# Performance work log

Measured on AMD Instinct MI355X. Metric: run time of the kernel, lower is better.

Reference implementation:

```python
import jax, jax.numpy as jnp
import numpy as np
import math

NUM_HEADS = 8


def setup_inputs() -> dict:
    key = jax.random.key(0)
    ks = jax.random.split(key, 6)
    b, s, e = 4, 2048, 512
    x = jax.random.normal(ks[0], (b, s, e), dtype=jnp.float32)
    # 0/1 adjacency matrix as float (it multiplies the scores in the module)
    adj = jax.random.randint(ks[1], (b, s, s), 0, 2).astype(jnp.float32)
    scale = 0.02
    Wqkv_w = jax.random.normal(ks[2], (3 * e, e), dtype=jnp.float32) * scale
    Wqkv_b = jax.random.normal(ks[3], (3 * e,), dtype=jnp.float32) * scale
    out_w = jax.random.normal(ks[4], (e, e), dtype=jnp.float32) * scale
    out_b = jax.random.normal(ks[5], (e,), dtype=jnp.float32) * scale
    return {"x": x, "adj": adj, "Wqkv_w": Wqkv_w, "Wqkv_b": Wqkv_b,
            "out_w": out_w, "out_b": out_b}


def reference(x, adj, Wqkv_w, Wqkv_b, out_w, out_b):
    b, s, e = x.shape
    h = NUM_HEADS
    d = e // h
    # fused qkv projection: (b, s, 3*e) -> (b, s, 3, h, d)
    qkv = (x @ Wqkv_w.T + Wqkv_b).reshape(b, s, 3, h, d)
    qkv = jnp.transpose(qkv, (2, 0, 3, 1, 4))  # (3, b, h, s, d)
    q, k, v = qkv[0], qkv[1], qkv[2]
    inv_sqrt_d = 1.0 / math.sqrt(d)
    scores = jnp.einsum('bhqd,bhkd->bhqk', q, k) * inv_sqrt_d
    scores = jnp.clip(scores * adj[:, None, :, :], -10000.0, 10000.0)
    attn = jax.nn.softmax(scores, axis=-1)
    out = jnp.einsum('bhqk,bhkd->bhqd', attn, v)
    out = jnp.transpose(out, (0, 2, 1, 3)).reshape(b, s, e)  # (b, s, h*d)
    return out @ out_w.T + out_b
```

## Files before the change

### kernel.cpp

```cpp
#include <hip/hip_runtime.h>


typedef __attribute__((ext_vector_type(8))) short bf16x8;
typedef __attribute__((ext_vector_type(4))) float f32x4;
typedef __attribute__((ext_vector_type(4))) unsigned short ushort4v;
typedef __attribute__((ext_vector_type(4))) _Float16 f16x4;

#if __has_builtin(__builtin_amdgcn_exp2f)
#define EXP2F(x) __builtin_amdgcn_exp2f(x)
#else
#define EXP2F(x) exp2f(x)
#endif

#define QSCALE 0.18033688011112042f

__device__ __forceinline__ unsigned short f2bf(float f) {
  unsigned int u = __float_as_uint(f);
  u += 0x7FFFu + ((u >> 16) & 1u);
  return (unsigned short)(u >> 16);
}
__device__ __forceinline__ unsigned short f2h(float f) {
  union { _Float16 h; unsigned short u; } cv;
  cv.h = (_Float16)f;
  return cv.u;
}

__global__ __launch_bounds__(256) void prep_k(const float* __restrict__ x,
                                              unsigned short* __restrict__ x_bf,
                                              const float* __restrict__ wqkv,
                                              unsigned short* __restrict__ wqkv_bf,
                                              const float* __restrict__ outw,
                                              unsigned short* __restrict__ outw_bf,
                                              const float* __restrict__ adj,
                                              unsigned long long* __restrict__ abits) {
  const int bid = blockIdx.x;
  if (bid < 5120) {
    const float* in; unsigned short* out; int i;
    if (bid < 4096) { in = x; out = x_bf; i = bid * 256 + threadIdx.x; }
    else if (bid < 4864) { in = wqkv; out = wqkv_bf; i = (bid - 4096) * 256 + threadIdx.x; }
    else { in = outw; out = outw_bf; i = (bid - 4864) * 256 + threadIdx.x; }
    float4 v = ((const float4*)in)[i];
    ushort4v o;
    o[0] = f2bf(v.x); o[1] = f2bf(v.y); o[2] = f2bf(v.z); o[3] = f2bf(v.w);
    ((ushort4v*)out)[i] = o;
  } else {
    const int gw = (bid - 5120) * 4 + (threadIdx.x >> 6);
    const int l = threadIdx.x & 63;
    const int b = gw >> 11, q = gw & 2047;
    const float* row = adj + ((size_t)b * 2048 + q) * 2048;
    unsigned long long* ob = abits + (size_t)b * 65536 + q;
#pragma unroll 4
    for (int kt = 0; kt < 32; ++kt) {
      const float v = row[kt * 64 + l];
      const unsigned long long m = __ballot(v != 0.f);
      if (l == 0) ob[(size_t)kt * 2048] = m;
    }
  }
}

template <int MODE>
__global__ __launch_bounds__(256) void gemm128_k(const unsigned short* __restrict__ A,
                                                 const unsigned short* __restrict__ Bt,
                                                 const float* __restrict__ bias, int Kdim,
                                                 int Ntiles, unsigned short* __restrict__ q_out,
                                                 unsigned short* __restrict__ k_out,
                                                 unsigned short* __restrict__ v_out,
                                                 float* __restrict__ f_out) {
  __shared__ unsigned short A_lds[128][40];
  __shared__ unsigned short B_lds[128][40];
  __shared__ unsigned short T_lds[64][136];

  const int t = threadIdx.x;
  const int lane = t & 63, w = t >> 6, ln = lane & 15, quad = lane >> 4;
  const int mt = blockIdx.x / Ntiles, nt = blockIdx.x % Ntiles;
  const int wm = (w >> 1) * 64, wn = (w & 1) * 64;
  const int strow = t >> 2, stcol = (t & 3) * 8;

  const size_t abase = (size_t)(mt * 128 + strow) * Kdim + stcol;
  const size_t bbase = (size_t)(nt * 128 + strow) * Kdim + stcol;

  f32x4 acc[4][4];
#pragma unroll
  for (int i = 0; i < 4; ++i)
#pragma unroll
    for (int j = 0; j < 4; ++j) acc[i][j] = (f32x4){0.f, 0.f, 0.f, 0.f};

  bf16x8 a0 = *(const bf16x8*)(A + abase);
  bf16x8 a1 = *(const bf16x8*)(A + abase + (size_t)64 * Kdim);
  bf16x8 b0 = *(const bf16x8*)(Bt + bbase);
  bf16x8 b1 = *(const bf16x8*)(Bt + bbase + (size_t)64 * Kdim);

  for (int kk = 0; kk < Kdim; kk += 32) {
    __syncthreads();
    *(bf16x8*)&A_lds[strow][stcol] = a0;
    *(bf16x8*)&A_lds[64 + strow][stcol] = a1;
    *(bf16x8*)&B_lds[strow][stcol] = b0;
    *(bf16x8*)&B_lds[64 + strow][stcol] = b1;
    __syncthreads();

    const int kn = (kk + 32) & (Kdim - 1);
    a0 = *(const bf16x8*)(A + abase + kn);
    a1 = *(const bf16x8*)(A + abase + (size_t)64 * Kdim + kn);
    b0 = *(const bf16x8*)(Bt + bbase + kn);
    b1 = *(const bf16x8*)(Bt + bbase + (size_t)64 * Kdim + kn);

    bf16x8 bfr[4];
#pragma unroll
    for (int nf = 0; nf < 4; ++nf) bfr[nf] = *(const bf16x8*)&B_lds[wn + nf * 16 + ln][quad * 8];
#pragma unroll
    for (int mf = 0; mf < 4; ++mf) {
      bf16x8 af = *(const bf16x8*)&A_lds[wm + mf * 16 + ln][quad * 8];
#pragma unroll
      for (int nf = 0; nf < 4; ++nf)
        acc[mf][nf] = __builtin_amdgcn_mfma_f32_16x16x32_bf16(af, bfr[nf], acc[mf][nf], 0, 0, 0);
    }
  }

  if (MODE == 0 && nt >= 8) {
    const int bb = mt >> 4, sq0 = (mt & 15) * 128;
#pragma unroll
    for (int half = 0; half < 2; ++half) {
      __syncthreads();
      if ((w & 1) == half) {
#pragma unroll
        for (int nf = 0; nf < 4; ++nf) {
          const float bv = bias[nt * 128 + half * 64 + nf * 16 + ln];
#pragma unroll
          for (int mf = 0; mf < 4; ++mf)
#pragma unroll
            for (int r = 0; r < 4; ++r)
              T_lds[nf * 16 + ln][wm + mf * 16 + quad * 4 + r] = f2h(acc[mf][nf][r] + bv);
        }
      }
      __syncthreads();
#pragma unroll
      for (int rep = 0; rep < 4; ++rep) {
        const int row = rep * 16 + (t >> 4), c = t & 15;
        const bf16x8 val = *(const bf16x8*)&T_lds[row][c * 8];
        const int hd = (nt - 8) * 128 + half * 64 + row;
        const int hh = hd >> 6, dd = hd & 63;
        *(bf16x8*)(v_out + ((size_t)(bb * 8 + hh) * 64 + dd) * 2048 + sq0 + c * 8) = val;
      }
    }
    return;
  }

#pragma unroll
  for (int mf = 0; mf < 4; ++mf) {
    const int m = mt * 128 + wm + mf * 16 + quad * 4;
#pragma unroll
    for (int nf = 0; nf < 4; ++nf) {
      const int n = nt * 128 + wn + nf * 16 + ln;
      const float bv = bias[n];
      if (MODE == 0) {
        const int hd = n & 511;
        const int hh = hd >> 6, dd = hd & 63;
        const int bb = m >> 11, sq = m & 2047;
        if (n < 512) {
#pragma unroll
          for (int r = 0; r < 4; ++r)
            q_out[((size_t)(bb * 8 + hh) * 2048 + sq + r) * 64 + dd] =
                f2bf((acc[mf][nf][r] + bv) * QSCALE);
        } else {
#pragma unroll
          for (int r = 0; r < 4; ++r)
            k_out[((size_t)(bb * 8 + hh) * 2048 + sq + r) * 64 + dd] = f2bf(acc[mf][nf][r] + bv);
        }
      } else {
#pragma unroll
        for (int r = 0; r < 4; ++r) f_out[(size_t)(m + r) * 512 + n] = acc[mf][nf][r] + bv;
      }
    }
  }
}

__global__ __launch_bounds__(256, 2) void attn_k(const unsigned short* __restrict__ Qg,
                                                 const unsigned short* __restrict__ Kg,
                                                 const unsigned short* __restrict__ Vg,
                                                 const unsigned long long* __restrict__ Mg,
                                                 unsigned short* __restrict__ Og) {
  __shared__ unsigned short K_lds[2][64][72];
  __shared__ unsigned short V_lds[2][64][72];
  __shared__ unsigned long long M_lds[2][128];

  const int t = threadIdx.x;
  const int w = t >> 6, lane = t & 63, ln = lane & 15, quad = lane >> 4;
  const int bh = blockIdx.x & 31, qt = blockIdx.x >> 5, bb = bh >> 3;
  const int sbase = qt * 128;

  const unsigned short* Qp = Qg + (size_t)bh * (2048 * 64);
  const unsigned short* Kp = Kg + (size_t)bh * (2048 * 64);
  const unsigned short* Vp = Vg + (size_t)bh * (64 * 2048);
  const unsigned long long* Mp = Mg + (size_t)bb * 65536 + sbase;

  bf16x8 qf[2][2];
#pragma unroll
  for (int qg = 0; qg < 2; ++qg) {
    const int qrow = sbase + w * 32 + qg * 16 + ln;
    qf[qg][0] = *(const bf16x8*)(Qp + (size_t)qrow * 64 + quad * 8);
    qf[qg][1] = *(const bf16x8*)(Qp + (size_t)qrow * 64 + 32 + quad * 8);
  }

  f32x4 acc_o[2][4];
#pragma unroll
  for (int qg = 0; qg < 2; ++qg)
#pragma unroll
    for (int dg = 0; dg < 4; ++dg) acc_o[qg][dg] = (f32x4){0.f, 0.f, 0.f, 0.f};
  float lsum[2] = {0.f, 0.f};

  const int strow = t >> 2;
  const int stcol = (t & 3) * 16;

  bf16x8 kr0 = *(const bf16x8*)(Kp + (size_t)strow * 64 + stcol);
  bf16x8 kr1 = *(const bf16x8*)(Kp + (size_t)strow * 64 + stcol + 8);
  bf16x8 vr0 = *(const bf16x8*)(Vp + (size_t)strow * 2048 + stcol);
  bf16x8 vr1 = *(const bf16x8*)(Vp + (size_t)strow * 2048 + stcol + 8);
  unsigned long long mreg = (w < 2) ? Mp[w * 64 + lane] : 0ull;
  *(bf16x8*)&K_lds[0][strow][stcol] = kr0;
  *(bf16x8*)&K_lds[0][strow][stcol + 8] = kr1;
  *(bf16x8*)&V_lds[0][strow][stcol] = vr0;
  *(bf16x8*)&V_lds[0][strow][stcol + 8] = vr1;
  if (w < 2) M_lds[0][w * 64 + lane] = mreg;
  __syncthreads();

  for (int kt = 0; kt < 32; ++kt) {
    const int cur = kt & 1, nxt = cur ^ 1;

    const int k0n = ((kt + 1) & 31) * 64;
    kr0 = *(const bf16x8*)(Kp + (size_t)(k0n + strow) * 64 + stcol);
    kr1 = *(const bf16x8*)(Kp + (size_t)(k0n + strow) * 64 + stcol + 8);
    vr0 = *(const bf16x8*)(Vp + (size_t)strow * 2048 + k0n + stcol);
    vr1 = *(const bf16x8*)(Vp + (size_t)strow * 2048 + k0n + stcol + 8);
    if (w < 2) mreg = Mp[((kt + 1) & 31) * 2048 + w * 64 + lane];

    f32x4 sc[2][4];
#pragma unroll
    for (int nf = 0; nf < 4; ++nf) {
      bf16x8 kf0 = *(const bf16x8*)&K_lds[cur][nf * 16 + ln][quad * 8];
      bf16x8 kf1 = *(const bf16x8*)&K_lds[cur][nf * 16 + ln][32 + quad * 8];
#pragma unroll
      for (int qg = 0; qg < 2; ++qg) {
        f32x4 z = (f32x4){0.f, 0.f, 0.f, 0.f};
        z = __builtin_amdgcn_mfma_f32_16x16x32_bf16(kf0, qf[qg][0], z, 0, 0, 0);
        sc[qg][nf] = __builtin_amdgcn_mfma_f32_16x16x32_bf16(kf1, qf[qg][1], z, 0, 0, 0);
      }
    }

    f16x4 pa[2][4];
#pragma unroll
    for (int qg = 0; qg < 2; ++qg) {
      const unsigned long long m64 = M_lds[cur][w * 32 + qg * 16 + ln];
#pragma unroll
      for (int nf = 0; nf < 4; ++nf) {
        const unsigned nib = (unsigned)(m64 >> (nf * 16 + quad * 4)) & 0xFu;
#pragma unroll
        for (int r = 0; r < 4; ++r) {
          const float s = (nib >> r) & 1u ? sc[qg][nf][r] : 0.f;
          const float p = EXP2F(s);
          lsum[qg] += p;
          pa[qg][nf][r] = (_Float16)p;
        }
      }
    }

#pragma unroll
    for (int ks = 0; ks < 4; ++ks) {
      f16x4 vf[4];
#pragma unroll
      for (int dg = 0; dg < 4; ++dg)
        vf[dg] = *(const f16x4*)&V_lds[cur][dg * 16 + ln][ks * 16 + quad * 4];
#pragma unroll
      for (int qg = 0; qg < 2; ++qg)
#pragma unroll
        for (int dg = 0; dg < 4; ++dg)
          acc_o[qg][dg] =
              __builtin_amdgcn_mfma_f32_16x16x16f16(pa[qg][ks], vf[dg], acc_o[qg][dg], 0, 0, 0);
    }

    if (kt < 31) {
      *(bf16x8*)&K_lds[nxt][strow][stcol] = kr0;
      *(bf16x8*)&K_lds[nxt][strow][stcol + 8] = kr1;
      *(bf16x8*)&V_lds[nxt][strow][stcol] = vr0;
      *(bf16x8*)&V_lds[nxt][strow][stcol + 8] = vr1;
      if (w < 2) M_lds[nxt][w * 64 + lane] = mreg;
      __syncthreads();
    }
  }

#pragma unroll
  for (int qg = 0; qg < 2; ++qg) {
    lsum[qg] += __shfl_xor(lsum[qg], 16);
    lsum[qg] += __shfl_xor(lsum[qg], 32);
    lsum[qg] = 1.0f / lsum[qg];
  }

  unsigned short* Op = Og + (size_t)bb * 2048 * 512 + (size_t)(bh & 7) * 64;
#pragma unroll
  for (int qg = 0; qg < 2; ++qg)
#pragma unroll
    for (int r = 0; r < 4; ++r) {
      const float inv = __shfl(lsum[qg], quad * 4 + r);
      const int sq = sbase + w * 32 + qg * 16 + quad * 4 + r;
#pragma unroll
      for (int dg = 0; dg < 4; ++dg)
        Op[(size_t)sq * 512 + dg * 16 + ln] = f2bf(acc_o[qg][dg][r] * inv);
    }
}

extern "C" void kernel_launch(void* const* d_in, const int* in_sizes, int n_in, void* d_out,
                              int out_size, void* d_ws, size_t ws_size, hipStream_t stream) {
  const float* x = (const float*)d_in[0];
  const float* adj = (const float*)d_in[1];
  const float* wqkv = (const float*)d_in[2];
  const float* bqkv = (const float*)d_in[3];
  const float* outw = (const float*)d_in[4];
  const float* outb = (const float*)d_in[5];
  float* out = (float*)d_out;

  char* ws = (char*)d_ws;
  unsigned short* x_bf = (unsigned short*)(ws);
  unsigned short* wqkv_bf = (unsigned short*)(ws + 8388608);
  unsigned short* outw_bf = (unsigned short*)(ws + 9961472);
  unsigned long long* abits = (unsigned long long*)(ws + 10485760);
  unsigned short* Qb = (unsigned short*)(ws + 27262976);
  unsigned short* Kb = (unsigned short*)(ws + 35651584);
  unsigned short* Vb = (unsigned short*)(ws + 44040192);
  unsigned short* Ob = (unsigned short*)(ws + 52428800);

  prep_k<<<7168, 256, 0, stream>>>(x, x_bf, wqkv, wqkv_bf, outw, outw_bf, adj, abits);

  gemm128_k<0><<<768, 256, 0, stream>>>(x_bf, wqkv_bf, bqkv, 512, 12, Qb, Kb, Vb, nullptr);

  attn_k<<<512, 256, 0, stream>>>(Qb, Kb, Vb, abits, Ob);

  gemm128_k<1><<<256, 256, 0, stream>>>(Ob, outw_bf, outb, 512, 4, nullptr, nullptr, nullptr, out);
}
```

Baseline: 239.2 us.

## Double-buffer GEMM LDS tiles and compute softmax row sums with MFMA

New measurement: 225.8 us. -5.6%, faster.

```diff
diff --git a/kernel.cpp b/kernel.cpp
--- a/kernel.cpp
+++ b/kernel.cpp
@@ -59,16 +59,17 @@
 }
 
 template <int MODE>
-__global__ __launch_bounds__(256) void gemm128_k(const unsigned short* __restrict__ A,
-                                                 const unsigned short* __restrict__ Bt,
-                                                 const float* __restrict__ bias, int Kdim,
-                                                 int Ntiles, unsigned short* __restrict__ q_out,
-                                                 unsigned short* __restrict__ k_out,
-                                                 unsigned short* __restrict__ v_out,
-                                                 float* __restrict__ f_out) {
-  __shared__ unsigned short A_lds[128][40];
-  __shared__ unsigned short B_lds[128][40];
-  __shared__ unsigned short T_lds[64][136];
+__global__ __launch_bounds__(256, 3) void gemm128_k(const unsigned short* __restrict__ A,
+                                                    const unsigned short* __restrict__ Bt,
+                                                    const float* __restrict__ bias, int Kdim,
+                                                    int Ntiles, unsigned short* __restrict__ q_out,
+                                                    unsigned short* __restrict__ k_out,
+                                                    unsigned short* __restrict__ v_out,
+                                                    float* __restrict__ f_out) {
+  __shared__ union {
+    struct { unsigned short A[2][128][40], B[2][128][40]; } s;
+    unsigned short T[64][136];
+  } u;
 
   const int t = threadIdx.x;
   const int lane = t & 63, w = t >> 6, ln = lane & 15, quad = lane >> 4;
@@ -89,16 +90,17 @@
   bf16x8 a1 = *(const bf16x8*)(A + abase + (size_t)64 * Kdim);
   bf16x8 b0 = *(const bf16x8*)(Bt + bbase);
   bf16x8 b1 = *(const bf16x8*)(Bt + bbase + (size_t)64 * Kdim);
-
-  for (int kk = 0; kk < Kdim; kk += 32) {
-    __syncthreads();
-    *(bf16x8*)&A_lds[strow][stcol] = a0;
-    *(bf16x8*)&A_lds[64 + strow][stcol] = a1;
-    *(bf16x8*)&B_lds[strow][stcol] = b0;
-    *(bf16x8*)&B_lds[64 + strow][stcol] = b1;
-    __syncthreads();
-
-    const int kn = (kk + 32) & (Kdim - 1);
+  *(bf16x8*)&u.s.A[0][strow][stcol] = a0;
+  *(bf16x8*)&u.s.A[0][64 + strow][stcol] = a1;
+  *(bf16x8*)&u.s.B[0][strow][stcol] = b0;
+  *(bf16x8*)&u.s.B[0][64 + strow][stcol] = b1;
+  __syncthreads();
+
+  const int iters = Kdim >> 5;
+  for (int it = 0; it < iters; ++it) {
+    const int cur = it & 1, nxt = cur ^ 1;
+
+    const int kn = ((it + 1) << 5) & (Kdim - 1);
     a0 = *(const bf16x8*)(A + abase + kn);
     a1 = *(const bf16x8*)(A + abase + (size_t)64 * Kdim + kn);
     b0 = *(const bf16x8*)(Bt + bbase + kn);
@@ -106,13 +108,22 @@
 
     bf16x8 bfr[4];
 #pragma unroll
-    for (int nf = 0; nf < 4; ++nf) bfr[nf] = *(const bf16x8*)&B_lds[wn + nf * 16 + ln][quad * 8];
+    for (int nf = 0; nf < 4; ++nf)
+      bfr[nf] = *(const bf16x8*)&u.s.B[cur][wn + nf * 16 + ln][quad * 8];
 #pragma unroll
     for (int mf = 0; mf < 4; ++mf) {
-      bf16x8 af = *(const bf16x8*)&A_lds[wm + mf * 16 + ln][quad * 8];
+      bf16x8 af = *(const bf16x8*)&u.s.A[cur][wm + mf * 16 + ln][quad * 8];
 #pragma unroll
       for (int nf = 0; nf < 4; ++nf)
         acc[mf][nf] = __builtin_amdgcn_mfma_f32_16x16x32_bf16(af, bfr[nf], acc[mf][nf], 0, 0, 0);
+    }
+
+    if (it + 1 < iters) {
+      *(bf16x8*)&u.s.A[nxt][strow][stcol] = a0;
+      *(bf16x8*)&u.s.A[nxt][64 + strow][stcol] = a1;
+      *(bf16x8*)&u.s.B[nxt][strow][stcol] = b0;
+      *(bf16x8*)&u.s.B[nxt][64 + strow][stcol] = b1;
+      __syncthreads();
     }
   }
 
@@ -129,14 +140,14 @@
           for (int mf = 0; mf < 4; ++mf)
 #pragma unroll
             for (int r = 0; r < 4; ++r)
-              T_lds[nf * 16 + ln][wm + mf * 16 + quad * 4 + r] = f2h(acc[mf][nf][r] + bv);
+              u.T[nf * 16 + ln][wm + mf * 16 + quad * 4 + r] = f2h(acc[mf][nf][r] + bv);
         }
       }
       __syncthreads();
 #pragma unroll
       for (int rep = 0; rep < 4; ++rep) {
         const int row = rep * 16 + (t >> 4), c = t & 15;
-        const bf16x8 val = *(const bf16x8*)&T_lds[row][c * 8];
+        const bf16x8 val = *(const bf16x8*)&u.T[row][c * 8];
         const int hd = (nt - 8) * 128 + half * 64 + row;
         const int hh = hd >> 6, dd = hd & 63;
         *(bf16x8*)(v_out + ((size_t)(bb * 8 + hh) * 64 + dd) * 2048 + sq0 + c * 8) = val;
@@ -201,12 +212,15 @@
     qf[qg][1] = *(const bf16x8*)(Qp + (size_t)qrow * 64 + 32 + quad * 8);
   }
 
+  const _Float16 one_h = (_Float16)((ln == 0) ? 1.0f : 0.0f);
+  const f16x4 vf_one = (f16x4){one_h, one_h, one_h, one_h};
+
   f32x4 acc_o[2][4];
 #pragma unroll
   for (int qg = 0; qg < 2; ++qg)
 #pragma unroll
     for (int dg = 0; dg < 4; ++dg) acc_o[qg][dg] = (f32x4){0.f, 0.f, 0.f, 0.f};
-  float lsum[2] = {0.f, 0.f};
+  f32x4 acc_1[2] = {(f32x4){0.f, 0.f, 0.f, 0.f}, (f32x4){0.f, 0.f, 0.f, 0.f}};
 
   const int strow = t >> 2;
   const int stcol = (t & 3) * 16;
@@ -246,6 +260,13 @@
       }
     }
 
+    f16x4 vfa[4][4];
+#pragma unroll
+    for (int ks = 0; ks < 4; ++ks)
+#pragma unroll
+      for (int dg = 0; dg < 4; ++dg)
+        vfa[ks][dg] = *(const f16x4*)&V_lds[cur][dg * 16 + ln][ks * 16 + quad * 4];
+
     f16x4 pa[2][4];
 #pragma unroll
     for (int qg = 0; qg < 2; ++qg) {
@@ -256,26 +277,21 @@
 #pragma unroll
         for (int r = 0; r < 4; ++r) {
           const float s = (nib >> r) & 1u ? sc[qg][nf][r] : 0.f;
-          const float p = EXP2F(s);
-          lsum[qg] += p;
-          pa[qg][nf][r] = (_Float16)p;
+          pa[qg][nf][r] = (_Float16)EXP2F(s);
         }
       }
     }
 
 #pragma unroll
-    for (int ks = 0; ks < 4; ++ks) {
-      f16x4 vf[4];
-#pragma unroll
-      for (int dg = 0; dg < 4; ++dg)
-        vf[dg] = *(const f16x4*)&V_lds[cur][dg * 16 + ln][ks * 16 + quad * 4];
-#pragma unroll
-      for (int qg = 0; qg < 2; ++qg)
+    for (int ks = 0; ks < 4; ++ks)
+#pragma unroll
+      for (int qg = 0; qg < 2; ++qg) {
 #pragma unroll
         for (int dg = 0; dg < 4; ++dg)
           acc_o[qg][dg] =
-              __builtin_amdgcn_mfma_f32_16x16x16f16(pa[qg][ks], vf[dg], acc_o[qg][dg], 0, 0, 0);
-    }
+              __builtin_amdgcn_mfma_f32_16x16x16f16(pa[qg][ks], vfa[ks][dg], acc_o[qg][dg], 0, 0, 0);
+        acc_1[qg] = __builtin_amdgcn_mfma_f32_16x16x16f16(pa[qg][ks], vf_one, acc_1[qg], 0, 0, 0);
+      }
 
     if (kt < 31) {
       *(bf16x8*)&K_lds[nxt][strow][stcol] = kr0;
@@ -287,19 +303,12 @@
     }
   }
 
-#pragma unroll
-  for (int qg = 0; qg < 2; ++qg) {
-    lsum[qg] += __shfl_xor(lsum[qg], 16);
-    lsum[qg] += __shfl_xor(lsum[qg], 32);
-    lsum[qg] = 1.0f / lsum[qg];
-  }
-
   unsigned short* Op = Og + (size_t)bb * 2048 * 512 + (size_t)(bh & 7) * 64;
 #pragma unroll
   for (int qg = 0; qg < 2; ++qg)
 #pragma unroll
     for (int r = 0; r < 4; ++r) {
-      const float inv = __shfl(lsum[qg], quad * 4 + r);
+      const float inv = 1.0f / __shfl(acc_1[qg][r], quad * 16);
       const int sq = sbase + w * 32 + qg * 16 + quad * 4 + r;
 #pragma unroll
       for (int dg = 0; dg < 4; ++dg)
```
